# Kernel optimization log

Measured on AMD Instinct MI355X. Metric: run time of the kernel, lower is better.

Reference implementation:

```python
import jax, jax.numpy as jnp
import numpy as np

N_LAYERS = 4
H = 16
LOOKBACK = 128  # cross_window
EPS = 1e-6
ROPE_BASE = 10000.0
NEG = jnp.float32(-1e30)


def rmsnorm(x, w):
    return x * jax.lax.rsqrt(jnp.mean(x * x, axis=-1, keepdims=True) + EPS) * w


def rope_cache(L, hd):
    inv = 1.0 / (ROPE_BASE ** (jnp.arange(0, hd, 2, dtype=jnp.float32) / hd))
    t = jnp.arange(L, dtype=jnp.float32)
    f = t[:, None] * inv[None, :]            # [L, hd/2]
    emb = jnp.concatenate([f, f], axis=-1)   # [L, hd]
    return jnp.cos(emb), jnp.sin(emb)


def apply_rope(x, cos, sin):
    # x: [B,H,L,d]; rotate-half convention
    d = x.shape[-1]
    x1, x2 = x[..., : d // 2], x[..., d // 2:]
    rot = jnp.concatenate([-x2, x1], axis=-1)
    return x * cos + rot * sin


def split_heads(x, n_heads):
    B, L, D = x.shape
    return x.reshape(B, L, n_heads, D // n_heads).transpose(0, 2, 1, 3)


def merge_heads(x):
    B, h, L, d = x.shape
    return x.transpose(0, 2, 1, 3).reshape(B, L, h * d)


def sdpa(q, k, v, bias):
    scale = q.shape[-1] ** -0.5
    s = jnp.einsum('bhqd,bhkd->bhqk', q, k) * scale + bias
    p = jax.nn.softmax(s, axis=-1)
    return jnp.einsum('bhqk,bhkd->bhqd', p, v)


def forward(x, memory, seg_ids, Wqkv, bqkv, Wo, bo, Wq_c, Wkv_c, Wo_c, Wg, Wu, Wd, n1, n2, n3, nf):
    B, L, D = x.shape
    S = memory.shape[1]
    hd = D // H
    cos, sin = rope_cache(L, hd)

    # causal additive mask [1,1,L,L]
    i = jnp.arange(L)
    causal_bias = jnp.where(i[None, :] <= i[:, None], 0.0, NEG)[None, None]

    # segment-causal sliding-window cross mask [B,1,L,S]:
    # token t may attend memory j with seg_id[t]-LOOKBACK < j <= seg_id[t]
    j = jnp.arange(S)
    allowed = (j[None, None, :] <= seg_ids[:, :, None]) & (j[None, None, :] > seg_ids[:, :, None] - LOOKBACK)
    cross_bias = jnp.where(allowed, 0.0, NEG)[:, None]  # [B,1,L,S]

    for l in range(N_LAYERS):
        # --- causal self-attn with RoPE ---
        h = rmsnorm(x, n1[l])
        qkv = h @ Wqkv[l].T + bqkv[l]                      # [B,L,3D]
        q, k, v = jnp.split(qkv, 3, axis=-1)
        q = apply_rope(split_heads(q, H), cos, sin)
        k = apply_rope(split_heads(k, H), cos, sin)
        v = split_heads(v, H)
        o = merge_heads(sdpa(q, k, v, causal_bias)) @ Wo[l].T + bo[l]
        x = x + o

        # --- segment-causal sliding-window cross-attn ---
        h2 = rmsnorm(x, n2[l])
        qc = split_heads(h2 @ Wq_c[l].T, H)
        kv = memory @ Wkv_c[l].T                           # [B,S,2D]
        kc, vc = jnp.split(kv, 2, axis=-1)
        kc, vc = split_heads(kc, H), split_heads(vc, H)
        oc = merge_heads(sdpa(qc, kc, vc, cross_bias)) @ Wo_c[l].T
        x = x + oc

        # --- SwiGLU FFN ---
        h3 = rmsnorm(x, n3[l])
        x = x + (jax.nn.silu(h3 @ Wg[l].T) * (h3 @ Wu[l].T)) @ Wd[l].T

    return rmsnorm(x, nf)


def setup_inputs() -> dict:
    key = jax.random.key(0)
    ks = jax.random.split(key, 16)
    B, L, S, D, F = 2, 2048, 256, 1024, 4096
    w = 0.02
    inp = {
        'x': jax.random.normal(ks[0], (B, L, D), jnp.float32),
        'memory': jax.random.normal(ks[1], (B, S, D), jnp.float32),
        'seg_ids': jnp.sort(jax.random.randint(ks[2], (B, L), 0, S), axis=-1),
        'Wqkv': jax.random.normal(ks[3], (N_LAYERS, 3 * D, D), jnp.float32) * w,
        'bqkv': jnp.zeros((N_LAYERS, 3 * D), jnp.float32),
        'Wo': jax.random.normal(ks[4], (N_LAYERS, D, D), jnp.float32) * w,
        'bo': jnp.zeros((N_LAYERS, D), jnp.float32),
        'Wq_c': jax.random.normal(ks[5], (N_LAYERS, D, D), jnp.float32) * w,
        'Wkv_c': jax.random.normal(ks[6], (N_LAYERS, 2 * D, D), jnp.float32) * w,
        'Wo_c': jax.random.normal(ks[7], (N_LAYERS, D, D), jnp.float32) * w,
        'Wg': jax.random.normal(ks[8], (N_LAYERS, F, D), jnp.float32) * w,
        'Wu': jax.random.normal(ks[9], (N_LAYERS, F, D), jnp.float32) * w,
        'Wd': jax.random.normal(ks[10], (N_LAYERS, D, F), jnp.float32) * w,
        'n1': jnp.ones((N_LAYERS, D), jnp.float32),
        'n2': jnp.ones((N_LAYERS, D), jnp.float32),
        'n3': jnp.ones((N_LAYERS, D), jnp.float32),
        'nf': jnp.ones((D,), jnp.float32),
    }
    return inp


def reference(x, memory, seg_ids, Wqkv, bqkv, Wo, bo, Wq_c, Wkv_c, Wo_c, Wg, Wu, Wd, n1, n2, n3, nf):
    return forward(x, memory, seg_ids, Wqkv, bqkv, Wo, bo, Wq_c, Wkv_c, Wo_c, Wg, Wu, Wd, n1, n2, n3, nf)
```

## Files before the change

### kernel.cpp

```cpp
#include <hip/hip_runtime.h>
#include <hip/hip_bf16.h>
#include <math.h>

#define N_LAYERS 4
#define NHEADS 16
#define LOOKBACK 128

typedef unsigned short ushort_t;
typedef __attribute__((ext_vector_type(8))) short short8;
typedef __attribute__((ext_vector_type(4))) float f32x4;

__device__ __forceinline__ ushort_t f2bf(float f) {
    union { float f; unsigned int u; } v; v.f = f;
    unsigned int r = (v.u + 0x7FFFu + ((v.u >> 16) & 1u)) >> 16;
    return (ushort_t)r;
}
__device__ __forceinline__ float bf2f(ushort_t s) {
    union { unsigned int u; float f; } v; v.u = ((unsigned int)s) << 16;
    return v.f;
}

__device__ __forceinline__ float blk_sum(float v, volatile float* red) {
#pragma unroll
    for (int o = 32; o > 0; o >>= 1) v += __shfl_down(v, o, 64);
    if ((threadIdx.x & 63) == 0) red[threadIdx.x >> 6] = v;
    __syncthreads();
    float r = red[0] + red[1] + red[2] + red[3];
    __syncthreads();
    return r;
}

__global__ __launch_bounds__(256) void f2b_k(const float* __restrict__ in,
                                             ushort_t* __restrict__ out, int n4) {
    int i = blockIdx.x * 256 + threadIdx.x;
    if (i >= n4) return;
    float4 v = *(const float4*)(in + (size_t)i * 4);
    ushort_t* o = out + (size_t)i * 4;
    o[0] = f2bf(v.x); o[1] = f2bf(v.y); o[2] = f2bf(v.z); o[3] = f2bf(v.w);
}

__global__ __launch_bounds__(256) void rmsnorm_bf(const float* __restrict__ x,
                                                  const float* __restrict__ w,
                                                  ushort_t* __restrict__ out, int D) {
    __shared__ float red[4];
    size_t row = blockIdx.x;
    const float* xr = x + row * D;
    float ss = 0.f;
    for (int i = threadIdx.x; i < D; i += 256) { float v = xr[i]; ss += v * v; }
    float tot = blk_sum(ss, red);
    float r = rsqrtf(tot / (float)D + 1e-6f);
    ushort_t* o = out + row * D;
    for (int i = threadIdx.x; i < D; i += 256) o[i] = f2bf(xr[i] * r * w[i]);
}

__global__ __launch_bounds__(256) void rmsnorm_k(const float* __restrict__ x,
                                                 const float* __restrict__ w,
                                                 float* __restrict__ out, int D) {
    __shared__ float red[4];
    size_t row = blockIdx.x;
    const float* xr = x + row * D;
    float ss = 0.f;
    for (int i = threadIdx.x; i < D; i += 256) { float v = xr[i]; ss += v * v; }
    float tot = blk_sum(ss, red);
    float r = rsqrtf(tot / (float)D + 1e-6f);
    float* o = out + row * D;
    for (int i = threadIdx.x; i < D; i += 256) o[i] = xr[i] * r * w[i];
}

#define GBM 128
#define GBN 128
#define GBK 32

__global__ __launch_bounds__(256) void gemm_bf16(
    const ushort_t* __restrict__ A, const ushort_t* __restrict__ Bw,
    void* __restrict__ Cout, const float* __restrict__ bias,
    const float* __restrict__ resid, const ushort_t* __restrict__ gate,
    int M, int N, int K, int out_bf16) {
    __shared__ ushort_t As[GBM * GBK];
    __shared__ ushort_t Bs[GBN * GBK];
    int tid = threadIdx.x;
    int wave = tid >> 6, lane = tid & 63;
    int nwg = gridDim.x * gridDim.y;
    int wg  = blockIdx.y * gridDim.x + blockIdx.x;
    int qq = nwg >> 3, rr = nwg & 7;
    int xcd = wg & 7, loc = wg >> 3;
    int swz = (xcd < rr ? xcd * (qq + 1) : rr * (qq + 1) + (xcd - rr) * qq) + loc;
    int bm = (swz / gridDim.x) * GBM, bn = (swz % gridDim.x) * GBN;
    int wm = (wave & 1) * 64, wn = (wave >> 1) * 64;
    int r4 = lane >> 2, c4 = lane & 3;
    int r = lane & 15, q = lane >> 4;

    f32x4 acc[4][4];
#pragma unroll
    for (int i = 0; i < 4; ++i)
#pragma unroll
        for (int j = 0; j < 4; ++j) acc[i][j] = (f32x4){0.f, 0.f, 0.f, 0.f};

    int srow = wave * 16 + r4;
    for (int k0 = 0; k0 < K; k0 += GBK) {
        const ushort_t* Ag = A + (size_t)(bm + srow) * K + k0 + c4 * 8;
        const ushort_t* Bg = Bw + (size_t)(bn + srow) * K + k0 + c4 * 8;
        __builtin_amdgcn_global_load_lds(
            (const __attribute__((address_space(1))) void*)Ag,
            (__attribute__((address_space(3))) void*)&As[wave * 16 * GBK],
            16, 0, 0);
        __builtin_amdgcn_global_load_lds(
            (const __attribute__((address_space(1))) void*)(Ag + (size_t)64 * K),
            (__attribute__((address_space(3))) void*)&As[(64 + wave * 16) * GBK],
            16, 0, 0);
        __builtin_amdgcn_global_load_lds(
            (const __attribute__((address_space(1))) void*)Bg,
            (__attribute__((address_space(3))) void*)&Bs[wave * 16 * GBK],
            16, 0, 0);
        __builtin_amdgcn_global_load_lds(
            (const __attribute__((address_space(1))) void*)(Bg + (size_t)64 * K),
            (__attribute__((address_space(3))) void*)&Bs[(64 + wave * 16) * GBK],
            16, 0, 0);
        __syncthreads();
        short8 af[4], bfr[4];
#pragma unroll
        for (int i = 0; i < 4; ++i)
            af[i] = *(const short8*)&As[(wm + 16 * i + r) * GBK + q * 8];
#pragma unroll
        for (int j = 0; j < 4; ++j)
            bfr[j] = *(const short8*)&Bs[(wn + 16 * j + r) * GBK + q * 8];
#pragma unroll
        for (int i = 0; i < 4; ++i)
#pragma unroll
            for (int j = 0; j < 4; ++j)
                acc[i][j] = __builtin_amdgcn_mfma_f32_16x16x32_bf16(
                    af[i], bfr[j], acc[i][j], 0, 0, 0);
        __syncthreads();
    }
#pragma unroll
    for (int i = 0; i < 4; ++i) {
#pragma unroll
        for (int j = 0; j < 4; ++j) {
            size_t n = (size_t)(bn + wn + 16 * j + r);
            float bn_v = bias ? bias[n] : 0.f;
#pragma unroll
            for (int t = 0; t < 4; ++t) {
                size_t m = (size_t)(bm + wm + 16 * i + q * 4 + t);
                size_t idx = m * N + n;
                float x = acc[i][j][t] + bn_v;
                if (gate) { float g = bf2f(gate[idx]); x *= g / (1.0f + __expf(-g)); }
                if (resid) x += resid[idx];
                if (out_bf16) ((ushort_t*)Cout)[idx] = f2bf(x);
                else ((float*)Cout)[idx] = x;
            }
        }
    }
}

__global__ void rope_k(ushort_t* __restrict__ qkv, int L, int total) {
    int idx = blockIdx.x * 256 + threadIdx.x;
    if (idx >= total) return;
    int d = idx & 31;
    int h = (idx >> 5) & 15;
    int bl = idx >> 9;
    int l = bl % L;
    float inv = exp2f(-(float)d * (13.2877123795f / 32.0f));
    float f = (float)l * inv;
    float s, c;
    sincosf(f, &s, &c);
    ushort_t* base = qkv + (size_t)bl * 3072 + h * 64 + d;
    float x1 = bf2f(base[0]), x2 = bf2f(base[32]);
    base[0]  = f2bf((x1 * c - x2 * s) * 0.125f);
    base[32] = f2bf((x2 * c + x1 * s) * 0.125f);
    ushort_t* kb = base + 1024;
    x1 = bf2f(kb[0]); x2 = bf2f(kb[32]);
    kb[0]  = f2bf(x1 * c - x2 * s);
    kb[32] = f2bf(x2 * c + x1 * s);
}

#define QB 128

__global__ __launch_bounds__(256) void self_attn_flash(
    const ushort_t* __restrict__ qkv, ushort_t* __restrict__ out, int L) {
    int lin = blockIdx.x + gridDim.x * (blockIdx.y + gridDim.y * blockIdx.z);
    int xcd = lin & 7, slot = lin >> 3;
    int qt = slot & 15;
    int grp = xcd + 8 * (slot >> 4);
    int h = grp & 15, b = grp >> 4;
    int q0 = qt * QB;

    __shared__ ushort_t Qs[QB * 72];
    __shared__ ushort_t Ks[64 * 72];
    __shared__ ushort_t VT[64 * 64];
    __shared__ ushort_t Ps[QB * 64];

    int tid = threadIdx.x;
    int wave = tid >> 6, lane = tid & 63;
    int g = lane >> 4, r = lane & 15;
    int lr2 = tid >> 1, lc2 = tid & 1;
    int lr = tid >> 2, lc = tid & 3;

    {
        const ushort_t* src = qkv + ((size_t)b * L + q0 + lr2) * 3072 + h * 64 + lc2 * 32;
        ushort_t* dst = &Qs[lr2 * 72 + lc2 * 32];
        *(short8*)(dst)      = *(const short8*)(src);
        *(short8*)(dst + 8)  = *(const short8*)(src + 8);
        *(short8*)(dst + 16) = *(const short8*)(src + 16);
        *(short8*)(dst + 24) = *(const short8*)(src + 24);
    }
    __syncthreads();
    short8 aq[2][2];
#pragma unroll
    for (int s = 0; s < 2; ++s)
#pragma unroll
        for (int c = 0; c < 2; ++c)
            aq[s][c] = *(const short8*)&Qs[(wave * 32 + s * 16 + r) * 72 + c * 32 + g * 8];

    const ushort_t* kvbase = qkv + ((size_t)b * L + lr) * 3072 + 1024 + h * 64 + lc * 16;
    short8 kreg0 = *(const short8*)(kvbase);
    short8 kreg1 = *(const short8*)(kvbase + 8);
    short8 vreg0 = *(const short8*)(kvbase + 1024);
    short8 vreg1 = *(const short8*)(kvbase + 1032);

    float m[2][4], lsum[2][4];
    f32x4 acc[2][4];
#pragma unroll
    for (int s = 0; s < 2; ++s)
#pragma unroll
        for (int t = 0; t < 4; ++t) { m[s][t] = -1e30f; lsum[s][t] = 0.f; }
#pragma unroll
    for (int s = 0; s < 2; ++s)
#pragma unroll
        for (int j = 0; j < 4; ++j) acc[s][j] = (f32x4){0.f, 0.f, 0.f, 0.f};

    int ktmax = 2 * qt + 1;
    for (int kt = 0; kt <= ktmax; ++kt) {
        __syncthreads();
        *(short8*)&Ks[lr * 72 + lc * 16]     = kreg0;
        *(short8*)&Ks[lr * 72 + lc * 16 + 8] = kreg1;
#pragma unroll
        for (int i = 0; i < 8; ++i) {
            int row0 = lc * 16 + i;
            int f0 = (row0 & 7) ^ ((row0 >> 4) & 3);
            VT[row0 * 64 + (((lr >> 3) ^ f0) << 3) + (lr & 7)] = (ushort_t)vreg0[i];
            int row1 = row0 + 8;
            int f1 = (row1 & 7) ^ ((row1 >> 4) & 3);
            VT[row1 * 64 + (((lr >> 3) ^ f1) << 3) + (lr & 7)] = (ushort_t)vreg1[i];
        }
        if (kt < ktmax) {
            const ushort_t* p = kvbase + (size_t)(kt + 1) * 64 * 3072;
            kreg0 = *(const short8*)(p);
            kreg1 = *(const short8*)(p + 8);
            vreg0 = *(const short8*)(p + 1024);
            vreg1 = *(const short8*)(p + 1032);
        }
        __syncthreads();

        int k0 = kt * 64;
        f32x4 s2[2][4];
#pragma unroll
        for (int s = 0; s < 2; ++s)
#pragma unroll
            for (int j = 0; j < 4; ++j) s2[s][j] = (f32x4){0.f, 0.f, 0.f, 0.f};
#pragma unroll
        for (int j = 0; j < 4; ++j)
#pragma unroll
            for (int c = 0; c < 2; ++c) {
                short8 bk = *(const short8*)&Ks[(16 * j + r) * 72 + c * 32 + g * 8];
                s2[0][j] = __builtin_amdgcn_mfma_f32_16x16x32_bf16(aq[0][c], bk, s2[0][j], 0, 0, 0);
                s2[1][j] = __builtin_amdgcn_mfma_f32_16x16x32_bf16(aq[1][c], bk, s2[1][j], 0, 0, 0);
            }

        if (kt >= ktmax - 1) {
#pragma unroll
            for (int s = 0; s < 2; ++s)
#pragma unroll
                for (int j = 0; j < 4; ++j) {
                    int k = k0 + 16 * j + r;
#pragma unroll
                    for (int t = 0; t < 4; ++t)
                        if (k > q0 + wave * 32 + s * 16 + 4 * g + t) s2[s][j][t] = -1e30f;
                }
        }

        float al[2][4];
#pragma unroll
        for (int s = 0; s < 2; ++s)
#pragma unroll
            for (int t = 0; t < 4; ++t) {
                float rm = fmaxf(fmaxf(s2[s][0][t], s2[s][1][t]), fmaxf(s2[s][2][t], s2[s][3][t]));
#pragma unroll
                for (int o = 8; o > 0; o >>= 1) rm = fmaxf(rm, __shfl_xor(rm, o, 16));
                float mn = fmaxf(m[s][t], rm);
                al[s][t] = __expf(m[s][t] - mn);
                m[s][t] = mn;
                float rs = 0.f;
#pragma unroll
                for (int j = 0; j < 4; ++j) {
                    float p = __expf(s2[s][j][t] - mn);
                    s2[s][j][t] = p;
                    rs += p;
                }
#pragma unroll
                for (int o = 8; o > 0; o >>= 1) rs += __shfl_xor(rs, o, 16);
                lsum[s][t] = lsum[s][t] * al[s][t] + rs;
            }

#pragma unroll
        for (int s = 0; s < 2; ++s)
#pragma unroll
            for (int j = 0; j < 4; ++j)
#pragma unroll
                for (int t = 0; t < 4; ++t) {
                    int row = wave * 32 + s * 16 + 4 * g + t;
                    int f = (row >> 1) & 7;
                    Ps[row * 64 + (((2 * j + (r >> 3)) ^ f) << 3) + (r & 7)] = f2bf(s2[s][j][t]);
                }
        short8 ap[2][2];
#pragma unroll
        for (int s = 0; s < 2; ++s) {
            int row = wave * 32 + s * 16 + r;
            int f = (row >> 1) & 7;
#pragma unroll
            for (int c = 0; c < 2; ++c)
                ap[s][c] = *(const short8*)&Ps[row * 64 + (((4 * c + g) ^ f) << 3)];
        }

#pragma unroll
        for (int s = 0; s < 2; ++s)
#pragma unroll
            for (int j = 0; j < 4; ++j)
#pragma unroll
                for (int t = 0; t < 4; ++t) acc[s][j][t] *= al[s][t];
#pragma unroll
        for (int j = 0; j < 4; ++j)
#pragma unroll
            for (int c = 0; c < 2; ++c) {
                int row = 16 * j + r;
                int ch = (4 * c + g) ^ (r & 7) ^ j;
                short8 bv = *(const short8*)&VT[row * 64 + (ch << 3)];
                acc[0][j] = __builtin_amdgcn_mfma_f32_16x16x32_bf16(ap[0][c], bv, acc[0][j], 0, 0, 0);
                acc[1][j] = __builtin_amdgcn_mfma_f32_16x16x32_bf16(ap[1][c], bv, acc[1][j], 0, 0, 0);
            }
    }

#pragma unroll
    for (int s = 0; s < 2; ++s)
#pragma unroll
        for (int t = 0; t < 4; ++t) {
            float invl = 1.0f / lsum[s][t];
            size_t orow = ((size_t)b * L + q0 + wave * 32 + s * 16 + 4 * g + t) * 1024 + h * 64;
#pragma unroll
            for (int j = 0; j < 4; ++j)
                out[orow + 16 * j + r] = f2bf(acc[s][j][t] * invl);
        }
}

#define AP 72

__global__ __launch_bounds__(256) void cross_attn_mfma(
    const ushort_t* __restrict__ qc, const ushort_t* __restrict__ kvc,
    const int* __restrict__ seg_ids, ushort_t* __restrict__ out, int L, int S) {
    int qt = blockIdx.x, h = blockIdx.y, b = blockIdx.z;
    int q0 = qt * 64;
    __shared__ ushort_t Qs[64 * AP];
    __shared__ ushort_t Ks[64 * AP];
    __shared__ ushort_t VT[64 * AP];
    __shared__ ushort_t Ps[64 * AP];
    __shared__ int segs[64];
    __shared__ int bounds[2];
    int tid = threadIdx.x;
    int wave = tid >> 6, lane = tid & 63;
    int g = lane >> 4, r = lane & 15;
    int lr = tid >> 2, lc = tid & 3;

    {
        const ushort_t* src = qc + ((size_t)b * L + q0 + lr) * 1024 + h * 64 + lc * 16;
        *(short8*)&Qs[lr * AP + lc * 16]     = *(const short8*)(src);
        *(short8*)&Qs[lr * AP + lc * 16 + 8] = *(const short8*)(src + 8);
    }
    if (tid < 64) segs[tid] = seg_ids[(size_t)b * L + q0 + tid];
    __syncthreads();
    if (wave == 0) {
        int v = segs[lane];
        int mn = v, mx = v;
#pragma unroll
        for (int o = 32; o > 0; o >>= 1) {
            mn = min(mn, __shfl_down(mn, o, 64));
            mx = max(mx, __shfl_down(mx, o, 64));
        }
        if (lane == 0) { bounds[0] = mn; bounds[1] = mx; }
    }
    int seg_t[4];
#pragma unroll
    for (int t = 0; t < 4; ++t) seg_t[t] = segs[wave * 16 + 4 * g + t];
    short8 aq[2];
#pragma unroll
    for (int c = 0; c < 2; ++c)
        aq[c] = *(const short8*)&Qs[(wave * 16 + r) * AP + c * 32 + g * 8];
    __syncthreads();
    int lo = bounds[0] - (LOOKBACK - 1); if (lo < 0) lo = 0;
    int t_lo = lo >> 6;
    int t_hi = bounds[1] >> 6;

    float m[4]    = {-1e30f, -1e30f, -1e30f, -1e30f};
    float lsum[4] = {0.f, 0.f, 0.f, 0.f};
    f32x4 acc[4];
#pragma unroll
    for (int j = 0; j < 4; ++j) acc[j] = (f32x4){0.f, 0.f, 0.f, 0.f};

    for (int kt = t_lo; kt <= t_hi; ++kt) {
        int k0 = kt * 64;
        __syncthreads();
        {
            const ushort_t* ksrc = kvc + ((size_t)b * S + k0 + lr) * 2048 + h * 64 + lc * 16;
            short8 k0v = *(const short8*)(ksrc);
            short8 k1v = *(const short8*)(ksrc + 8);
            *(short8*)&Ks[lr * AP + lc * 16]     = k0v;
            *(short8*)&Ks[lr * AP + lc * 16 + 8] = k1v;
            const ushort_t* vsrc = ksrc + 1024;
            short8 v0v = *(const short8*)(vsrc);
            short8 v1v = *(const short8*)(vsrc + 8);
#pragma unroll
            for (int i = 0; i < 8; ++i) {
                VT[(lc * 16 + i) * AP + lr]     = (ushort_t)v0v[i];
                VT[(lc * 16 + 8 + i) * AP + lr] = (ushort_t)v1v[i];
            }
        }
        __syncthreads();

        f32x4 s[4];
#pragma unroll
        for (int j = 0; j < 4; ++j) s[j] = (f32x4){0.f, 0.f, 0.f, 0.f};
#pragma unroll
        for (int j = 0; j < 4; ++j)
#pragma unroll
            for (int c = 0; c < 2; ++c) {
                short8 bk = *(const short8*)&Ks[(16 * j + r) * AP + c * 32 + g * 8];
                s[j] = __builtin_amdgcn_mfma_f32_16x16x32_bf16(aq[c], bk, s[j], 0, 0, 0);
            }

#pragma unroll
        for (int j = 0; j < 4; ++j) {
            int k = k0 + 16 * j + r;
#pragma unroll
            for (int t = 0; t < 4; ++t) {
                float v = s[j][t] * 0.125f;
                if (k > seg_t[t] || k <= seg_t[t] - LOOKBACK) v = -1e30f;
                s[j][t] = v;
            }
        }

        float al[4];
#pragma unroll
        for (int t = 0; t < 4; ++t) {
            float rm = fmaxf(fmaxf(s[0][t], s[1][t]), fmaxf(s[2][t], s[3][t]));
#pragma unroll
            for (int o = 8; o > 0; o >>= 1) rm = fmaxf(rm, __shfl_xor(rm, o, 16));
            float mn = fmaxf(m[t], rm);
            al[t] = __expf(m[t] - mn);
            m[t] = mn;
            float rs = 0.f;
#pragma unroll
            for (int j = 0; j < 4; ++j) {
                float p = __expf(s[j][t] - mn);
                s[j][t] = p;
                rs += p;
            }
#pragma unroll
            for (int o = 8; o > 0; o >>= 1) rs += __shfl_xor(rs, o, 16);
            lsum[t] = lsum[t] * al[t] + rs;
        }

        ushort_t* pw = &Ps[wave * 16 * AP];
#pragma unroll
        for (int j = 0; j < 4; ++j)
#pragma unroll
            for (int t = 0; t < 4; ++t)
                pw[(4 * g + t) * AP + 16 * j + r] = f2bf(s[j][t]);
        short8 ap[2];
#pragma unroll
        for (int c = 0; c < 2; ++c)
            ap[c] = *(const short8*)&pw[r * AP + c * 32 + g * 8];

#pragma unroll
        for (int j = 0; j < 4; ++j) {
#pragma unroll
            for (int t = 0; t < 4; ++t) acc[j][t] *= al[t];
#pragma unroll
            for (int c = 0; c < 2; ++c) {
                short8 bv = *(const short8*)&VT[(16 * j + r) * AP + c * 32 + g * 8];
                acc[j] = __builtin_amdgcn_mfma_f32_16x16x32_bf16(ap[c], bv, acc[j], 0, 0, 0);
            }
        }
    }

#pragma unroll
    for (int t = 0; t < 4; ++t) {
        float invl = 1.0f / lsum[t];
        size_t orow = ((size_t)b * L + q0 + wave * 16 + 4 * g + t) * 1024 + h * 64;
#pragma unroll
        for (int j = 0; j < 4; ++j)
            out[orow + 16 * j + r] = f2bf(acc[j][t] * invl);
    }
}

extern "C" void kernel_launch(void* const* d_in, const int* in_sizes, int n_in,
                              void* d_out, int out_size, void* d_ws, size_t ws_size,
                              hipStream_t stream) {
    const int B = 2, L = 2048, S = 256, D = 1024, F = 4096;
    const int BL = B * L;
    const float* x_in   = (const float*)d_in[0];
    const float* memory = (const float*)d_in[1];
    const int*   seg    = (const int*)d_in[2];
    const float* Wqkv = (const float*)d_in[3];
    const float* bqkv = (const float*)d_in[4];
    const float* Wo   = (const float*)d_in[5];
    const float* bo   = (const float*)d_in[6];
    const float* Wq_c = (const float*)d_in[7];
    const float* Wkv_c= (const float*)d_in[8];
    const float* Wo_c = (const float*)d_in[9];
    const float* Wg   = (const float*)d_in[10];
    const float* Wu   = (const float*)d_in[11];
    const float* Wd   = (const float*)d_in[12];
    const float* n1   = (const float*)d_in[13];
    const float* n2   = (const float*)d_in[14];
    const float* n3   = (const float*)d_in[15];
    const float* nf   = (const float*)d_in[16];

    char* ws = (char*)d_ws;
    size_t off = 0;
    float* X     = (float*)(ws + off); off += (size_t)BL * D * 4;
    float* QKV   = (float*)(ws + off); off += (size_t)BL * 3 * D * 4;
    float* KVC   = (float*)(ws + off); off += (size_t)B * S * 2 * D * 4;
    ushort_t* Hn  = (ushort_t*)(ws + off); off += (size_t)BL * D * 2;
    ushort_t* Abf = (ushort_t*)(ws + off); off += (size_t)BL * D * 2;
    ushort_t* Mb  = (ushort_t*)(ws + off); off += (size_t)B * S * D * 2;
    ushort_t* Wb  = (ushort_t*)(ws + off); off += (size_t)F * D * 2;
    ushort_t* QKVb = (ushort_t*)QKV;
    ushort_t* Qcb  = (ushort_t*)QKV;
    ushort_t* KVCb = (ushort_t*)KVC;
    ushort_t* Gg = (ushort_t*)QKV;

    hipMemcpyAsync(X, x_in, (size_t)BL * D * sizeof(float), hipMemcpyDeviceToDevice, stream);

    dim3 blk(256);
    f2b_k<<<(B * S * D / 4 + 255) / 256, blk, 0, stream>>>(memory, Mb, B * S * D / 4);

    for (int l = 0; l < N_LAYERS; ++l) {
        rmsnorm_bf<<<BL, blk, 0, stream>>>(X, n1 + (size_t)l * D, Hn, D);
        f2b_k<<<(3 * D * D / 4 + 255) / 256, blk, 0, stream>>>(
            Wqkv + (size_t)l * 3 * D * D, Wb, 3 * D * D / 4);
        gemm_bf16<<<dim3(3 * D / GBN, BL / GBM), blk, 0, stream>>>(
            Hn, Wb, QKVb, bqkv + (size_t)l * 3 * D, nullptr, nullptr, BL, 3 * D, D, 1);
        int total = BL * NHEADS * 32;
        rope_k<<<(total + 255) / 256, blk, 0, stream>>>(QKVb, L, total);
        self_attn_flash<<<dim3(L / QB, NHEADS, B), blk, 0, stream>>>(QKVb, Abf, L);
        f2b_k<<<(D * D / 4 + 255) / 256, blk, 0, stream>>>(
            Wo + (size_t)l * D * D, Wb, D * D / 4);
        gemm_bf16<<<dim3(D / GBN, BL / GBM), blk, 0, stream>>>(
            Abf, Wb, X, bo + (size_t)l * D, X, nullptr, BL, D, D, 0);
        rmsnorm_bf<<<BL, blk, 0, stream>>>(X, n2 + (size_t)l * D, Hn, D);
        f2b_k<<<(D * D / 4 + 255) / 256, blk, 0, stream>>>(
            Wq_c + (size_t)l * D * D, Wb, D * D / 4);
        gemm_bf16<<<dim3(D / GBN, BL / GBM), blk, 0, stream>>>(
            Hn, Wb, Qcb, nullptr, nullptr, nullptr, BL, D, D, 1);
        f2b_k<<<(2 * D * D / 4 + 255) / 256, blk, 0, stream>>>(
            Wkv_c + (size_t)l * 2 * D * D, Wb, 2 * D * D / 4);
        gemm_bf16<<<dim3(2 * D / GBN, B * S / GBM), blk, 0, stream>>>(
            Mb, Wb, KVCb, nullptr, nullptr, nullptr, B * S, 2 * D, D, 1);
        cross_attn_mfma<<<dim3(L / 64, NHEADS, B), blk, 0, stream>>>(
            Qcb, KVCb, seg, Abf, L, S);
        f2b_k<<<(D * D / 4 + 255) / 256, blk, 0, stream>>>(
            Wo_c + (size_t)l * D * D, Wb, D * D / 4);
        gemm_bf16<<<dim3(D / GBN, BL / GBM), blk, 0, stream>>>(
            Abf, Wb, X, nullptr, X, nullptr, BL, D, D, 0);
        rmsnorm_bf<<<BL, blk, 0, stream>>>(X, n3 + (size_t)l * D, Hn, D);
        f2b_k<<<(F * D / 4 + 255) / 256, blk, 0, stream>>>(
            Wg + (size_t)l * F * D, Wb, F * D / 4);
        gemm_bf16<<<dim3(F / GBN, BL / GBM), blk, 0, stream>>>(
            Hn, Wb, Gg, nullptr, nullptr, nullptr, BL, F, D, 1);
        f2b_k<<<(F * D / 4 + 255) / 256, blk, 0, stream>>>(
            Wu + (size_t)l * F * D, Wb, F * D / 4);
        gemm_bf16<<<dim3(F / GBN, BL / GBM), blk, 0, stream>>>(
            Hn, Wb, Gg, nullptr, nullptr, Gg, BL, F, D, 1);
        f2b_k<<<(D * F / 4 + 255) / 256, blk, 0, stream>>>(
            Wd + (size_t)l * D * F, Wb, D * F / 4);
        gemm_bf16<<<dim3(D / GBN, BL / GBM), blk, 0, stream>>>(
            Gg, Wb, X, nullptr, X, nullptr, BL, D, F, 0);
    }
    rmsnorm_k<<<BL, blk, 0, stream>>>(X, nf, (float*)d_out, D);
}
```

Measured before the change: 2.864 ms.

## Double-buffer LDS in GEMM and self-attention, prefetching next tile during compute

The GEMM now keeps two LDS buffers and issues the global-to-LDS loads for the next K tile before computing on the current one, using vmcnt waits and raw s_barrier instead of two __syncthreads per step. The self-attention kernel double-buffers its K/V LDS tiles, dropping one barrier per iteration, and raises wave priority with s_setprio around its MFMA blocks. The goal is to hide global load latency and cut synchronisation. In exchange it doubles the LDS footprint, which may lower occupancy, and relies on hand-placed waitcnt/barrier ordering being correct.

```diff
diff --git a/kernel.cpp b/kernel.cpp
--- a/kernel.cpp
+++ b/kernel.cpp
@@ -71,13 +71,34 @@
 #define GBN 128
 #define GBK 32
 
+#define STAGE_GEMM(kk, buf) do {                                               \
+    const ushort_t* Ag_ = A + (size_t)(bm + srow) * K + (kk) + c4 * 8;         \
+    const ushort_t* Bg_ = Bw + (size_t)(bn + srow) * K + (kk) + c4 * 8;        \
+    __builtin_amdgcn_global_load_lds(                                          \
+        (const __attribute__((address_space(1))) void*)Ag_,                    \
+        (__attribute__((address_space(3))) void*)&As[buf][wave * 16 * GBK],    \
+        16, 0, 0);                                                             \
+    __builtin_amdgcn_global_load_lds(                                          \
+        (const __attribute__((address_space(1))) void*)(Ag_ + (size_t)64 * K), \
+        (__attribute__((address_space(3))) void*)&As[buf][(64 + wave * 16) * GBK], \
+        16, 0, 0);                                                             \
+    __builtin_amdgcn_global_load_lds(                                          \
+        (const __attribute__((address_space(1))) void*)Bg_,                    \
+        (__attribute__((address_space(3))) void*)&Bs[buf][wave * 16 * GBK],    \
+        16, 0, 0);                                                             \
+    __builtin_amdgcn_global_load_lds(                                          \
+        (const __attribute__((address_space(1))) void*)(Bg_ + (size_t)64 * K), \
+        (__attribute__((address_space(3))) void*)&Bs[buf][(64 + wave * 16) * GBK], \
+        16, 0, 0);                                                             \
+} while (0)
+
 __global__ __launch_bounds__(256) void gemm_bf16(
     const ushort_t* __restrict__ A, const ushort_t* __restrict__ Bw,
     void* __restrict__ Cout, const float* __restrict__ bias,
     const float* __restrict__ resid, const ushort_t* __restrict__ gate,
     int M, int N, int K, int out_bf16) {
-    __shared__ ushort_t As[GBM * GBK];
-    __shared__ ushort_t Bs[GBN * GBK];
+    __shared__ ushort_t As[2][GBM * GBK];
+    __shared__ ushort_t Bs[2][GBN * GBK];
     int tid = threadIdx.x;
     int wave = tid >> 6, lane = tid & 63;
     int nwg = gridDim.x * gridDim.y;
@@ -97,40 +118,33 @@
         for (int j = 0; j < 4; ++j) acc[i][j] = (f32x4){0.f, 0.f, 0.f, 0.f};
 
     int srow = wave * 16 + r4;
-    for (int k0 = 0; k0 < K; k0 += GBK) {
-        const ushort_t* Ag = A + (size_t)(bm + srow) * K + k0 + c4 * 8;
-        const ushort_t* Bg = Bw + (size_t)(bn + srow) * K + k0 + c4 * 8;
-        __builtin_amdgcn_global_load_lds(
-            (const __attribute__((address_space(1))) void*)Ag,
-            (__attribute__((address_space(3))) void*)&As[wave * 16 * GBK],
-            16, 0, 0);
-        __builtin_amdgcn_global_load_lds(
-            (const __attribute__((address_space(1))) void*)(Ag + (size_t)64 * K),
-            (__attribute__((address_space(3))) void*)&As[(64 + wave * 16) * GBK],
-            16, 0, 0);
-        __builtin_amdgcn_global_load_lds(
-            (const __attribute__((address_space(1))) void*)Bg,
-            (__attribute__((address_space(3))) void*)&Bs[wave * 16 * GBK],
-            16, 0, 0);
-        __builtin_amdgcn_global_load_lds(
-            (const __attribute__((address_space(1))) void*)(Bg + (size_t)64 * K),
-            (__attribute__((address_space(3))) void*)&Bs[(64 + wave * 16) * GBK],
-            16, 0, 0);
-        __syncthreads();
+    int nt = K / GBK;
+    STAGE_GEMM(0, 0);
+    for (int t = 0; t < nt; ++t) {
+        int cur = t & 1;
+        if (t + 1 < nt) {
+            STAGE_GEMM((t + 1) * GBK, cur ^ 1);
+            asm volatile("s_waitcnt vmcnt(4)" ::: "memory");
+        } else {
+            asm volatile("s_waitcnt vmcnt(0)" ::: "memory");
+        }
+        __builtin_amdgcn_s_barrier();
+        __builtin_amdgcn_sched_barrier(0);
         short8 af[4], bfr[4];
 #pragma unroll
         for (int i = 0; i < 4; ++i)
-            af[i] = *(const short8*)&As[(wm + 16 * i + r) * GBK + q * 8];
+            af[i] = *(const short8*)&As[cur][(wm + 16 * i + r) * GBK + q * 8];
 #pragma unroll
         for (int j = 0; j < 4; ++j)
-            bfr[j] = *(const short8*)&Bs[(wn + 16 * j + r) * GBK + q * 8];
+            bfr[j] = *(const short8*)&Bs[cur][(wn + 16 * j + r) * GBK + q * 8];
 #pragma unroll
         for (int i = 0; i < 4; ++i)
 #pragma unroll
             for (int j = 0; j < 4; ++j)
                 acc[i][j] = __builtin_amdgcn_mfma_f32_16x16x32_bf16(
                     af[i], bfr[j], acc[i][j], 0, 0, 0);
-        __syncthreads();
+        __builtin_amdgcn_s_barrier();
+        __builtin_amdgcn_sched_barrier(0);
     }
 #pragma unroll
     for (int i = 0; i < 4; ++i) {
@@ -185,8 +199,8 @@
     int q0 = qt * QB;
 
     __shared__ ushort_t Qs[QB * 72];
-    __shared__ ushort_t Ks[64 * 72];
-    __shared__ ushort_t VT[64 * 64];
+    __shared__ ushort_t Ks[2][64 * 72];
+    __shared__ ushort_t VT[2][64 * 64];
     __shared__ ushort_t Ps[QB * 64];
 
     int tid = threadIdx.x;
@@ -230,18 +244,23 @@
 
     int ktmax = 2 * qt + 1;
     for (int kt = 0; kt <= ktmax; ++kt) {
-        __syncthreads();
-        *(short8*)&Ks[lr * 72 + lc * 16]     = kreg0;
-        *(short8*)&Ks[lr * 72 + lc * 16 + 8] = kreg1;
+        int cb = kt & 1;
+        ushort_t* Kc = &Ks[cb][0];
+        ushort_t* Vc = &VT[cb][0];
+        *(short8*)&Kc[lr * 72 + lc * 16]     = kreg0;
+        *(short8*)&Kc[lr * 72 + lc * 16 + 8] = kreg1;
 #pragma unroll
         for (int i = 0; i < 8; ++i) {
             int row0 = lc * 16 + i;
             int f0 = (row0 & 7) ^ ((row0 >> 4) & 3);
-            VT[row0 * 64 + (((lr >> 3) ^ f0) << 3) + (lr & 7)] = (ushort_t)vreg0[i];
+            Vc[row0 * 64 + (((lr >> 3) ^ f0) << 3) + (lr & 7)] = (ushort_t)vreg0[i];
             int row1 = row0 + 8;
             int f1 = (row1 & 7) ^ ((row1 >> 4) & 3);
-            VT[row1 * 64 + (((lr >> 3) ^ f1) << 3) + (lr & 7)] = (ushort_t)vreg1[i];
-        }
+            Vc[row1 * 64 + (((lr >> 3) ^ f1) << 3) + (lr & 7)] = (ushort_t)vreg1[i];
+        }
+        asm volatile("s_waitcnt lgkmcnt(0)" ::: "memory");
+        __builtin_amdgcn_s_barrier();
+        __builtin_amdgcn_sched_barrier(0);
         if (kt < ktmax) {
             const ushort_t* p = kvbase + (size_t)(kt + 1) * 64 * 3072;
             kreg0 = *(const short8*)(p);
@@ -249,7 +268,6 @@
             vreg0 = *(const short8*)(p + 1024);
             vreg1 = *(const short8*)(p + 1032);
         }
-        __syncthreads();
 
         int k0 = kt * 64;
         f32x4 s2[2][4];
@@ -257,14 +275,16 @@
         for (int s = 0; s < 2; ++s)
 #pragma unroll
             for (int j = 0; j < 4; ++j) s2[s][j] = (f32x4){0.f, 0.f, 0.f, 0.f};
+        __builtin_amdgcn_s_setprio(1);
 #pragma unroll
         for (int j = 0; j < 4; ++j)
 #pragma unroll
             for (int c = 0; c < 2; ++c) {
-                short8 bk = *(const short8*)&Ks[(16 * j + r) * 72 + c * 32 + g * 8];
+                short8 bk = *(const short8*)&Kc[(16 * j + r) * 72 + c * 32 + g * 8];
                 s2[0][j] = __builtin_amdgcn_mfma_f32_16x16x32_bf16(aq[0][c], bk, s2[0][j], 0, 0, 0);
                 s2[1][j] = __builtin_amdgcn_mfma_f32_16x16x32_bf16(aq[1][c], bk, s2[1][j], 0, 0, 0);
             }
+        __builtin_amdgcn_s_setprio(0);
 
         if (kt >= ktmax - 1) {
 #pragma unroll
@@ -327,16 +347,18 @@
             for (int j = 0; j < 4; ++j)
 #pragma unroll
                 for (int t = 0; t < 4; ++t) acc[s][j][t] *= al[s][t];
+        __builtin_amdgcn_s_setprio(1);
 #pragma unroll
         for (int j = 0; j < 4; ++j)
 #pragma unroll
             for (int c = 0; c < 2; ++c) {
                 int row = 16 * j + r;
                 int ch = (4 * c + g) ^ (r & 7) ^ j;
-                short8 bv = *(const short8*)&VT[row * 64 + (ch << 3)];
+                short8 bv = *(const short8*)&Vc[row * 64 + (ch << 3)];
                 acc[0][j] = __builtin_amdgcn_mfma_f32_16x16x32_bf16(ap[0][c], bv, acc[0][j], 0, 0, 0);
                 acc[1][j] = __builtin_amdgcn_mfma_f32_16x16x32_bf16(ap[1][c], bv, acc[1][j], 0, 0, 0);
             }
+        __builtin_amdgcn_s_setprio(0);
     }
 
 #pragma unroll
```

New measurement: 2.718 ms. -5.1%, faster.
